# Kernel optimization log

Hardware: AMD Instinct MI355X
Metric: run time of the kernel (lower is better)

The kernel has to match this reference:

```python
import jax, jax.numpy as jnp
import numpy as np

DIM = 768
NH = 12
HD = DIM // NH
HIDDEN = 4 * DIM
Z_SIZE = (8, 8)
X_SIZE = (16, 16)
SCALE = HD ** -0.5
LN_EPS = 1e-5


def _rel_index(q_size, kv_size):
    hq, wq = q_size
    hk, wk = kv_size
    cq = np.stack(np.meshgrid(np.arange(hq), np.arange(wq), indexing='ij'), -1).reshape(-1, 2)
    ck = np.stack(np.meshgrid(np.arange(hk), np.arange(wk), indexing='ij'), -1).reshape(-1, 2)
    rel = cq[:, None, :] - ck[None, :, :]  # (Lq, Lk, 2)
    rel[..., 0] += hk - 1
    rel[..., 1] += wk - 1
    return jnp.asarray(rel[..., 0] * (wq + wk - 1) + rel[..., 1])  # (Lq, Lk)

ZX_IDX = _rel_index(Z_SIZE, X_SIZE)  # (64, 256)
XZ_IDX = _rel_index(X_SIZE, Z_SIZE)  # (256, 64)


def _ln(v, g, b):
    m = jnp.mean(v, -1, keepdims=True)
    var = jnp.var(v, -1, keepdims=True)
    return (v - m) * jax.lax.rsqrt(var + LN_EPS) * g + b


def _cross_attn(q_in, kv_in, qw, qb, kvw, kvb, pw, pb, rpb, idx):
    B, Lq, D = q_in.shape
    Lk = kv_in.shape[1]
    q = (q_in @ qw.T + qb).reshape(B, Lq, NH, HD).transpose(0, 2, 1, 3)  # (B,H,Lq,hd)
    kv = (kv_in @ kvw.T + kvb).reshape(B, Lk, 2, NH, HD).transpose(2, 0, 3, 1, 4)
    k, v = kv[0], kv[1]  # (B,H,Lk,hd)
    bias = rpb[idx].transpose(2, 0, 1)  # (H,Lq,Lk)
    attn = jnp.einsum('bhqd,bhkd->bhqk', q, k) * SCALE + bias[None]
    attn = jax.nn.softmax(attn, axis=-1)
    o = jnp.einsum('bhqk,bhkd->bhqd', attn, v).transpose(0, 2, 1, 3).reshape(B, Lq, D)
    return o @ pw.T + pb


def _mlp(v, w1, b1, w2, b2):
    return jax.nn.gelu(v @ w1.T + b1, approximate=False) @ w2.T + b2


def setup_inputs() -> dict:
    key = jax.random.key(0)
    ks = jax.random.split(key, 24)
    w = lambda k, s: jax.random.normal(k, s, jnp.float32) * 0.02
    TBL = (Z_SIZE[0] + X_SIZE[0] - 1) * (Z_SIZE[1] + X_SIZE[1] - 1)  # 529
    return {
        'z': jax.random.normal(ks[0], (64, 64, DIM), jnp.float32),
        'x': jax.random.normal(ks[1], (64, 256, DIM), jnp.float32),
        'z_ln1_g': jnp.ones((DIM,), jnp.float32), 'z_ln1_b': jnp.zeros((DIM,), jnp.float32),
        'x_ln1_g': jnp.ones((DIM,), jnp.float32), 'x_ln1_b': jnp.zeros((DIM,), jnp.float32),
        'zx_qw': w(ks[2], (DIM, DIM)), 'zx_qb': jnp.zeros((DIM,), jnp.float32),
        'zx_kvw': w(ks[3], (2 * DIM, DIM)), 'zx_kvb': jnp.zeros((2 * DIM,), jnp.float32),
        'zx_pw': w(ks[4], (DIM, DIM)), 'zx_pb': jnp.zeros((DIM,), jnp.float32),
        'zx_rpb': w(ks[5], (TBL, NH)),
        'xz_qw': w(ks[6], (DIM, DIM)), 'xz_qb': jnp.zeros((DIM,), jnp.float32),
        'xz_kvw': w(ks[7], (2 * DIM, DIM)), 'xz_kvb': jnp.zeros((2 * DIM,), jnp.float32),
        'xz_pw': w(ks[8], (DIM, DIM)), 'xz_pb': jnp.zeros((DIM,), jnp.float32),
        'xz_rpb': w(ks[9], (TBL, NH)),
        'z_ln2_g': jnp.ones((DIM,), jnp.float32), 'z_ln2_b': jnp.zeros((DIM,), jnp.float32),
        'z_fc1_w': w(ks[10], (HIDDEN, DIM)), 'z_fc1_b': jnp.zeros((HIDDEN,), jnp.float32),
        'z_fc2_w': w(ks[11], (DIM, HIDDEN)), 'z_fc2_b': jnp.zeros((DIM,), jnp.float32),
        'x_ln2_g': jnp.ones((DIM,), jnp.float32), 'x_ln2_b': jnp.zeros((DIM,), jnp.float32),
        'x_fc1_w': w(ks[12], (HIDDEN, DIM)), 'x_fc1_b': jnp.zeros((HIDDEN,), jnp.float32),
        'x_fc2_w': w(ks[13], (DIM, HIDDEN)), 'x_fc2_b': jnp.zeros((DIM,), jnp.float32),
    }


def reference(z, x, z_ln1_g, z_ln1_b, x_ln1_g, x_ln1_b,
              zx_qw, zx_qb, zx_kvw, zx_kvb, zx_pw, zx_pb, zx_rpb,
              xz_qw, xz_qb, xz_kvw, xz_kvb, xz_pw, xz_pb, xz_rpb,
              z_ln2_g, z_ln2_b, z_fc1_w, z_fc1_b, z_fc2_w, z_fc2_b,
              x_ln2_g, x_ln2_b, x_fc1_w, x_fc1_b, x_fc2_w, x_fc2_b):
    zn = _ln(z, z_ln1_g, z_ln1_b)
    xn = _ln(x, x_ln1_g, x_ln1_b)
    z_attn = _cross_attn(zn, xn, zx_qw, zx_qb, zx_kvw, zx_kvb, zx_pw, zx_pb, zx_rpb, ZX_IDX)
    x_attn = _cross_attn(xn, zn, xz_qw, xz_qb, xz_kvw, xz_kvb, xz_pw, xz_pb, xz_rpb, XZ_IDX)
    z2 = z + z_attn
    z2 = z2 + _mlp(_ln(z2, z_ln2_g, z_ln2_b), z_fc1_w, z_fc1_b, z_fc2_w, z_fc2_b)
    x2 = x + x_attn
    x2 = x2 + _mlp(_ln(x2, x_ln2_g, x_ln2_b), x_fc1_w, x_fc1_b, x_fc2_w, x_fc2_b)
    return (z2, x2)
```

## Files before the change

kernel.cpp:

```cpp
#include <hip/hip_runtime.h>
#include <math.h>

typedef unsigned short u16;
typedef unsigned int u32;
typedef __attribute__((ext_vector_type(8))) short bf16x8;
typedef __attribute__((ext_vector_type(4))) float f32x4;
typedef __attribute__((ext_vector_type(4))) u16 u16x4;

__device__ __forceinline__ u16 f2bf(float f) {
  u32 u = __builtin_bit_cast(u32, f);
  u32 r = (u + 0x7fffu + ((u >> 16) & 1u)) >> 16;
  return (u16)r;
}

__device__ __forceinline__ float gelu_f(float v) {
  float u = 1.5957691216057308f * v * (1.0f + 0.044715f * v * v);
  return v / (1.0f + __expf(-u));
}

__device__ __forceinline__ void async16(const void* g, void* l) {
  __builtin_amdgcn_global_load_lds(
      (__attribute__((address_space(1))) void*)(unsigned long long)(const char*)g,
      (__attribute__((address_space(3))) void*)l, 16, 0, 0);
}

#define SCHED0 __builtin_amdgcn_sched_barrier(0)
#define BARRIER __builtin_amdgcn_s_barrier()

struct Conv10 {
  const float* src[10];
  u16* dst[10];
  int n[10];
};

__global__ __launch_bounds__(256) void convert10(Conv10 a) {
  const int seg = blockIdx.y;
  const long i = ((long)blockIdx.x * 256 + threadIdx.x) * 4;
  if (i >= a.n[seg]) return;
  float4 v = *(const float4*)&a.src[seg][i];
  u16x4 o;
  o.x = f2bf(v.x); o.y = f2bf(v.y); o.z = f2bf(v.z); o.w = f2bf(v.w);
  *(u16x4*)&a.dst[seg][i] = o;
}

__global__ __launch_bounds__(256) void pack_bias(
    const float* __restrict__ zq, const float* __restrict__ zkv,
    const float* __restrict__ xq, const float* __restrict__ xkv,
    float* __restrict__ bz, float* __restrict__ bx)
{
  const int i = blockIdx.x * 256 + threadIdx.x;
  if (i >= 2304) return;
  bz[i] = (i < 768) ? zq[i] : zkv[i - 768];
  bx[i] = (i < 768) ? xq[i] : xkv[i - 768];
}

__global__ __launch_bounds__(256) void ln_dual(
    const float* __restrict__ in1, const float* __restrict__ g1, const float* __restrict__ b1,
    u16* __restrict__ out1, int rows1,
    const float* __restrict__ in2, const float* __restrict__ g2, const float* __restrict__ b2,
    u16* __restrict__ out2)
{
  const int w = threadIdx.x >> 6;
  const int lane = threadIdx.x & 63;
  const int row = blockIdx.x * 4 + w;
  const float* in; const float* gg; const float* bb; u16* out;
  if (row < rows1) { in = in1 + (size_t)row * 768; gg = g1; bb = b1; out = out1 + (size_t)row * 768; }
  else { const int r2 = row - rows1; in = in2 + (size_t)r2 * 768; gg = g2; bb = b2; out = out2 + (size_t)r2 * 768; }

  float4 v0 = *(const float4*)&in[lane * 4];
  float4 v1 = *(const float4*)&in[lane * 4 + 256];
  float4 v2 = *(const float4*)&in[lane * 4 + 512];
  float s = v0.x + v0.y + v0.z + v0.w + v1.x + v1.y + v1.z + v1.w + v2.x + v2.y + v2.z + v2.w;
  float s2 = v0.x*v0.x + v0.y*v0.y + v0.z*v0.z + v0.w*v0.w
           + v1.x*v1.x + v1.y*v1.y + v1.z*v1.z + v1.w*v1.w
           + v2.x*v2.x + v2.y*v2.y + v2.z*v2.z + v2.w*v2.w;
#pragma unroll
  for (int m = 1; m <= 32; m <<= 1) { s += __shfl_xor(s, m); s2 += __shfl_xor(s2, m); }
  const float mean = s * (1.0f / 768.0f);
  const float var = s2 * (1.0f / 768.0f) - mean * mean;
  const float rs = rsqrtf(var + 1e-5f);

#define LNSTORE(V, OFFS) { \
    float4 gv = *(const float4*)&gg[lane * 4 + OFFS]; \
    float4 bv = *(const float4*)&bb[lane * 4 + OFFS]; \
    u16x4 o; \
    o.x = f2bf((V.x - mean) * rs * gv.x + bv.x); \
    o.y = f2bf((V.y - mean) * rs * gv.y + bv.y); \
    o.z = f2bf((V.z - mean) * rs * gv.z + bv.z); \
    o.w = f2bf((V.w - mean) * rs * gv.w + bv.w); \
    *(u16x4*)&out[lane * 4 + OFFS] = o; }
  LNSTORE(v0, 0)
  LNSTORE(v1, 256)
  LNSTORE(v2, 512)
#undef LNSTORE
}

template<int EPI>
__device__ __forceinline__ void gemm5_core(
    const u16* __restrict__ A, const u16* __restrict__ W,
    const float* __restrict__ bias, const float* __restrict__ res,
    void* __restrict__ outp, long row0, long col0, int N, int K)
{
  __shared__ __align__(16) u16 As[3][256 * 32];
  __shared__ __align__(16) u16 Bs[3][128 * 32];

  const int tid = threadIdx.x;
  const int lane = tid & 63;
  const int w = tid >> 6;
  const int wm = w >> 1;
  const int wn = w & 1;

  const u16* gA[4];
  const u16* gB[2];
#pragma unroll
  for (int l = 0; l < 4; ++l) {
    const int e = l * 256 + tid;
    const int r = e >> 2, sl = e & 3;
    gA[l] = A + (row0 + r) * (long)K + ((sl ^ ((r >> 1) & 3)) * 8);
  }
#pragma unroll
  for (int l = 0; l < 2; ++l) {
    const int e = l * 256 + tid;
    const int r = e >> 2, sl = e & 3;
    gB[l] = W + (col0 + r) * (long)K + ((sl ^ ((r >> 1) & 3)) * 8);
  }

  const int fr = lane & 15;
  const int g = lane >> 4;

  f32x4 acc[8][4];
#pragma unroll
  for (int m = 0; m < 8; ++m)
#pragma unroll
    for (int n = 0; n < 4; ++n) acc[m][n] = (f32x4){0.f, 0.f, 0.f, 0.f};

  auto stage = [&](u16* ab, u16* bb, long ko) {
#pragma unroll
    for (int l = 0; l < 4; ++l) async16(gA[l] + ko, &ab[(l * 256 + tid) * 8]);
#pragma unroll
    for (int l = 0; l < 2; ++l) async16(gB[l] + ko, &bb[(l * 256 + tid) * 8]);
  };

  const int nt = K / 32;
  u16 *a0 = &As[0][0], *a1 = &As[1][0], *a2 = &As[2][0];
  u16 *b0 = &Bs[0][0], *b1 = &Bs[1][0], *b2 = &Bs[2][0];

  stage(a0, b0, 0);
  stage(a1, b1, 32);
  SCHED0;
  asm volatile("s_waitcnt vmcnt(6)" ::: "memory");
  BARRIER;
  SCHED0;

  for (int t = 0; t < nt; ++t) {
    if (t + 2 < nt) stage(a2, b2, (long)(t + 2) * 32);
    SCHED0;
    bf16x8 bfr[4];
#pragma unroll
    for (int n = 0; n < 4; ++n) {
      const int r = wn * 64 + n * 16 + fr;
      bfr[n] = *(const bf16x8*)&b0[r * 32 + ((g ^ ((r >> 1) & 3)) * 8)];
    }
    __builtin_amdgcn_s_setprio(1);
#pragma unroll
    for (int m = 0; m < 8; ++m) {
      const int r = wm * 128 + m * 16 + fr;
      bf16x8 af = *(const bf16x8*)&a0[r * 32 + ((g ^ ((r >> 1) & 3)) * 8)];
#pragma unroll
      for (int n = 0; n < 4; ++n)
        acc[m][n] = __builtin_amdgcn_mfma_f32_16x16x32_bf16(af, bfr[n], acc[m][n], 0, 0, 0);
    }
    __builtin_amdgcn_s_setprio(0);
    SCHED0;
    if (t + 2 < nt) {
      asm volatile("s_waitcnt vmcnt(6) lgkmcnt(0)" ::: "memory");
    } else if (t + 1 < nt) {
      asm volatile("s_waitcnt vmcnt(0) lgkmcnt(0)" ::: "memory");
    }
    if (t + 1 < nt) { BARRIER; SCHED0; }
    u16* ta = a0; a0 = a1; a1 = a2; a2 = ta;
    u16* tb = b0; b0 = b1; b1 = b2; b2 = tb;
  }

  float bv[4];
#pragma unroll
  for (int n = 0; n < 4; ++n) bv[n] = bias[col0 + wn * 64 + n * 16 + fr];
#pragma unroll
  for (int m = 0; m < 8; ++m) {
#pragma unroll
    for (int j = 0; j < 4; ++j) {
      const long row = row0 + wm * 128 + m * 16 + g * 4 + j;
      const long base = row * N + col0 + wn * 64 + fr;
#pragma unroll
      for (int n = 0; n < 4; ++n) {
        float v = acc[m][n][j] + bv[n];
        if constexpr (EPI == 0) {
          ((u16*)outp)[base + n * 16] = f2bf(v);
        } else if constexpr (EPI == 1) {
          ((u16*)outp)[base + n * 16] = f2bf(gelu_f(v));
        } else {
          ((float*)outp)[base + n * 16] = v + res[base + n * 16];
        }
      }
    }
  }
}

template<int EPI>
__global__ __launch_bounds__(256, 2) void gemm5(
    const u16* __restrict__ A, const u16* __restrict__ W,
    const float* __restrict__ bias, const float* __restrict__ res,
    void* __restrict__ outp, int M, int N, int K)
{
  int flat = blockIdx.y * gridDim.x + blockIdx.x;
  const int nwg = gridDim.x * gridDim.y;
  if ((nwg & 7) == 0) flat = (flat & 7) * (nwg >> 3) + (flat >> 3);
  const int bx = flat % gridDim.x;
  const int by = flat / gridDim.x;
  gemm5_core<EPI>(A, W, bias, res, outp, (long)by * 256, (long)bx * 128, N, K);
}

template<int EPI>
__global__ __launch_bounds__(256, 2) void gemm5f(
    const u16* __restrict__ A0, const u16* __restrict__ W0,
    const float* __restrict__ bias0, const float* __restrict__ res0, void* __restrict__ out0,
    const u16* __restrict__ A1, const u16* __restrict__ W1,
    const float* __restrict__ bias1, const float* __restrict__ res1, void* __restrict__ out1,
    int Y0, int N, int K)
{
  int flat = blockIdx.y * gridDim.x + blockIdx.x;
  const int nwg = gridDim.x * gridDim.y;
  if ((nwg & 7) == 0) flat = (flat & 7) * (nwg >> 3) + (flat >> 3);
  const int bx = flat % gridDim.x;
  const int by = flat / gridDim.x;
  if (by < Y0) {
    gemm5_core<EPI>(A0, W0, bias0, res0, out0, (long)by * 256, (long)bx * 128, N, K);
  } else {
    gemm5_core<EPI>(A1, W1, bias1, res1, out1, (long)(by - Y0) * 256, (long)bx * 128, N, K);
  }
}

template<int LQ>
__device__ __forceinline__ int rel_index(int q, int k) {
  if constexpr (LQ == 64) {
    const int qh = q >> 3, qw = q & 7, kh = k >> 4, kw = k & 15;
    return (qh - kh + 15) * 23 + (qw - kw + 15);
  } else {
    const int qh = q >> 4, qw = q & 15, kh = k >> 3, kw = k & 7;
    return (qh - kh + 7) * 23 + (qw - kw + 7);
  }
}

template<int LQ, int LK>
__global__ __launch_bounds__(256) void attn_kernel(
    const u16* __restrict__ Q, int qs, const u16* __restrict__ KV, int ks,
    const float* __restrict__ rpb, u16* __restrict__ O)
{
  constexpr int MT = LQ / 64;
  constexpr int NT = LK / 16;
  constexpr int KSPV = LK / 32;

  __shared__ __align__(16) u16 Qs[LQ * 64];
  __shared__ __align__(16) u16 Ks[LK * 64];
  __shared__ __align__(16) u16 Vt[64 * LK];
  __shared__ __align__(16) u16 Ps[LQ * LK];
  __shared__ float bias_s[529];

  const int h = blockIdx.x;
  const int b = blockIdx.y;
  const int tid = threadIdx.x;
  const int lane = tid & 63;
  const int w = tid >> 6;

  for (int i = tid; i < 529; i += 256) bias_s[i] = rpb[i * 12 + h];

#pragma unroll
  for (int it = 0; it < LQ * 8 / 256; ++it) {
    const int s = it * 256 + tid;
    const int r = s >> 3, sl2 = s & 7;
    bf16x8 v = *(const bf16x8*)&Q[(size_t)(b * LQ + r) * qs + h * 64 + sl2 * 8];
    *(bf16x8*)&Qs[r * 64 + ((sl2 ^ (r & 7)) * 8)] = v;
  }
#pragma unroll
  for (int it = 0; it < LK * 8 / 256; ++it) {
    const int s = it * 256 + tid;
    const int r = s >> 3, sl2 = s & 7;
    bf16x8 v = *(const bf16x8*)&KV[(size_t)(b * LK + r) * ks + h * 64 + sl2 * 8];
    *(bf16x8*)&Ks[r * 64 + ((sl2 ^ (r & 7)) * 8)] = v;
  }
#pragma unroll
  for (int it = 0; it < LK * 8 / 256; ++it) {
    const int s = it * 256 + tid;
    const int r = s >> 3, sl2 = s & 7;
    const int d0 = sl2 * 8;
    bf16x8 v = *(const bf16x8*)&KV[(size_t)(b * LK + r) * ks + 768 + h * 64 + d0];
#pragma unroll
    for (int j = 0; j < 8; ++j) {
      const int d = d0 + j;
      Vt[d * LK + (((r >> 3) ^ (d & 7)) * 8) + (r & 7)] = (u16)v[j];
    }
  }
  __syncthreads();

  const int fr = lane & 15;
  const int g = lane >> 4;
  const int qbase = w * MT * 16;

  f32x4 sacc[MT][NT];
#pragma unroll
  for (int mt = 0; mt < MT; ++mt)
#pragma unroll
    for (int nt = 0; nt < NT; ++nt) sacc[mt][nt] = (f32x4){0.f, 0.f, 0.f, 0.f};

#pragma unroll
  for (int mt = 0; mt < MT; ++mt) {
    const int qr = qbase + mt * 16 + fr;
    bf16x8 aq0 = *(const bf16x8*)&Qs[qr * 64 + (((0 + g) ^ (qr & 7)) * 8)];
    bf16x8 aq1 = *(const bf16x8*)&Qs[qr * 64 + (((4 + g) ^ (qr & 7)) * 8)];
#pragma unroll
    for (int nt = 0; nt < NT; ++nt) {
      const int kr = nt * 16 + fr;
      bf16x8 bk0 = *(const bf16x8*)&Ks[kr * 64 + (((0 + g) ^ (kr & 7)) * 8)];
      bf16x8 bk1 = *(const bf16x8*)&Ks[kr * 64 + (((4 + g) ^ (kr & 7)) * 8)];
      sacc[mt][nt] = __builtin_amdgcn_mfma_f32_16x16x32_bf16(aq0, bk0, sacc[mt][nt], 0, 0, 0);
      sacc[mt][nt] = __builtin_amdgcn_mfma_f32_16x16x32_bf16(aq1, bk1, sacc[mt][nt], 0, 0, 0);
    }
  }

#pragma unroll
  for (int mt = 0; mt < MT; ++mt) {
#pragma unroll
    for (int reg = 0; reg < 4; ++reg) {
      const int q = qbase + mt * 16 + g * 4 + reg;
      float mx = -3.0e38f;
#pragma unroll
      for (int nt = 0; nt < NT; ++nt) {
        const int k = nt * 16 + fr;
        float s = sacc[mt][nt][reg] * 0.125f + bias_s[rel_index<LQ>(q, k)];
        sacc[mt][nt][reg] = s;
        mx = fmaxf(mx, s);
      }
      mx = fmaxf(mx, __shfl_xor(mx, 1));
      mx = fmaxf(mx, __shfl_xor(mx, 2));
      mx = fmaxf(mx, __shfl_xor(mx, 4));
      mx = fmaxf(mx, __shfl_xor(mx, 8));
      float sum = 0.f;
#pragma unroll
      for (int nt = 0; nt < NT; ++nt) {
        float p = __expf(sacc[mt][nt][reg] - mx);
        sacc[mt][nt][reg] = p;
        sum += p;
      }
      sum += __shfl_xor(sum, 1);
      sum += __shfl_xor(sum, 2);
      sum += __shfl_xor(sum, 4);
      sum += __shfl_xor(sum, 8);
      const float inv = 1.0f / sum;
#pragma unroll
      for (int nt = 0; nt < NT; ++nt) {
        const int k = nt * 16 + fr;
        Ps[q * LK + (((k >> 3) ^ (q & 7)) * 8) + (k & 7)] = f2bf(sacc[mt][nt][reg] * inv);
      }
    }
  }
  __syncthreads();

  f32x4 oacc[MT][4];
#pragma unroll
  for (int mt = 0; mt < MT; ++mt)
#pragma unroll
    for (int n = 0; n < 4; ++n) oacc[mt][n] = (f32x4){0.f, 0.f, 0.f, 0.f};

#pragma unroll
  for (int mt = 0; mt < MT; ++mt) {
    const int pr = qbase + mt * 16 + fr;
#pragma unroll
    for (int ks2 = 0; ks2 < KSPV; ++ks2) {
      bf16x8 ap = *(const bf16x8*)&Ps[pr * LK + (((ks2 * 4 + g) ^ (pr & 7)) * 8)];
#pragma unroll
      for (int n = 0; n < 4; ++n) {
        const int d = n * 16 + fr;
        bf16x8 bvv = *(const bf16x8*)&Vt[d * LK + (((ks2 * 4 + g) ^ (d & 7)) * 8)];
        oacc[mt][n] = __builtin_amdgcn_mfma_f32_16x16x32_bf16(ap, bvv, oacc[mt][n], 0, 0, 0);
      }
    }
  }

#pragma unroll
  for (int mt = 0; mt < MT; ++mt)
#pragma unroll
    for (int n = 0; n < 4; ++n)
#pragma unroll
      for (int reg = 0; reg < 4; ++reg) {
        const int q = qbase + mt * 16 + g * 4 + reg;
        const int d = n * 16 + fr;
        O[(size_t)(b * LQ + q) * 768 + h * 64 + d] = f2bf(oacc[mt][n][reg]);
      }
}

extern "C" void kernel_launch(void* const* d_in, const int* in_sizes, int n_in,
                              void* d_out, int out_size, void* d_ws, size_t ws_size,
                              hipStream_t stream)
{
  const float* z      = (const float*)d_in[0];
  const float* x      = (const float*)d_in[1];
  const float* zln1g  = (const float*)d_in[2];
  const float* zln1b  = (const float*)d_in[3];
  const float* xln1g  = (const float*)d_in[4];
  const float* xln1b  = (const float*)d_in[5];
  const float* zx_qw  = (const float*)d_in[6];
  const float* zx_qb  = (const float*)d_in[7];
  const float* zx_kvw = (const float*)d_in[8];
  const float* zx_kvb = (const float*)d_in[9];
  const float* zx_pw  = (const float*)d_in[10];
  const float* zx_pb  = (const float*)d_in[11];
  const float* zx_rpb = (const float*)d_in[12];
  const float* xz_qw  = (const float*)d_in[13];
  const float* xz_qb  = (const float*)d_in[14];
  const float* xz_kvw = (const float*)d_in[15];
  const float* xz_kvb = (const float*)d_in[16];
  const float* xz_pw  = (const float*)d_in[17];
  const float* xz_pb  = (const float*)d_in[18];
  const float* xz_rpb = (const float*)d_in[19];
  const float* zln2g  = (const float*)d_in[20];
  const float* zln2b  = (const float*)d_in[21];
  const float* zfc1w  = (const float*)d_in[22];
  const float* zfc1b  = (const float*)d_in[23];
  const float* zfc2w  = (const float*)d_in[24];
  const float* zfc2b  = (const float*)d_in[25];
  const float* xln2g  = (const float*)d_in[26];
  const float* xln2b  = (const float*)d_in[27];
  const float* xfc1w  = (const float*)d_in[28];
  const float* xfc1b  = (const float*)d_in[29];
  const float* xfc2w  = (const float*)d_in[30];
  const float* xfc2b  = (const float*)d_in[31];

  float* out = (float*)d_out;
  float* z2 = out;
  float* x2 = out + 3145728;

  char* ws = (char*)d_ws;
  size_t off = 0;
  auto take = [&](size_t bytes) {
    char* p = ws + off;
    off += (bytes + 255) & ~(size_t)255;
    return p;
  };
  u16* w_zn   = (u16*)take(1769472 * 2);
  u16* w_xn   = (u16*)take(1769472 * 2);
  u16* w_zx_p = (u16*)take(589824 * 2);
  u16* w_xz_p = (u16*)take(589824 * 2);
  u16* w_zfc1 = (u16*)take(2359296 * 2);
  u16* w_zfc2 = (u16*)take(2359296 * 2);
  u16* w_xfc1 = (u16*)take(2359296 * 2);
  u16* w_xfc2 = (u16*)take(2359296 * 2);
  float* b_zn = (float*)take(2304 * 4);
  float* b_xn = (float*)take(2304 * 4);
  u16* regA   = (u16*)take(31457280);

  const size_t need_full = off + 125829120;
  const bool full = (ws_size >= need_full);
  u16* regB = (u16*)take(full ? 125829120 : 94371840);

  u16* zn    = regA;
  u16* xn    = regA + 3145728;
  u16* qkv_z = regB;
  u16* qkv_x = regB + 9437184;
  u16* ao_z  = zn;
  u16* ao_x  = xn;
  u16* z2n   = zn;
  u16* x2n   = xn;
  u16* hz    = regB;
  u16* hx    = regB + 12582912;

  Conv10 c;
  c.src[0] = zx_qw;  c.dst[0] = w_zn;           c.n[0] = 589824;
  c.src[1] = xz_kvw; c.dst[1] = w_zn + 589824;  c.n[1] = 1179648;
  c.src[2] = xz_qw;  c.dst[2] = w_xn;           c.n[2] = 589824;
  c.src[3] = zx_kvw; c.dst[3] = w_xn + 589824;  c.n[3] = 1179648;
  c.src[4] = zx_pw;  c.dst[4] = w_zx_p;         c.n[4] = 589824;
  c.src[5] = xz_pw;  c.dst[5] = w_xz_p;         c.n[5] = 589824;
  c.src[6] = zfc1w;  c.dst[6] = w_zfc1;         c.n[6] = 2359296;
  c.src[7] = zfc2w;  c.dst[7] = w_zfc2;         c.n[7] = 2359296;
  c.src[8] = xfc1w;  c.dst[8] = w_xfc1;         c.n[8] = 2359296;
  c.src[9] = xfc2w;  c.dst[9] = w_xfc2;         c.n[9] = 2359296;
  convert10<<<dim3(2304, 10), 256, 0, stream>>>(c);
  pack_bias<<<9, 256, 0, stream>>>(zx_qb, xz_kvb, xz_qb, zx_kvb, b_zn, b_xn);

  ln_dual<<<5120, 256, 0, stream>>>(z, zln1g, zln1b, zn, 4096, x, xln1g, xln1b, xn);

  gemm5f<0><<<dim3(18, 80), 256, 0, stream>>>(
      zn, w_zn, b_zn, nullptr, qkv_z,
      xn, w_xn, b_xn, nullptr, qkv_x, 16, 2304, 768);

  attn_kernel<64, 256><<<dim3(12, 64), 256, 0, stream>>>(qkv_z, 2304, qkv_x + 768, 2304, zx_rpb, ao_z);
  attn_kernel<256, 64><<<dim3(12, 64), 256, 0, stream>>>(qkv_x, 2304, qkv_z + 768, 2304, xz_rpb, ao_x);

  gemm5f<2><<<dim3(6, 80), 256, 0, stream>>>(
      ao_z, w_zx_p, zx_pb, z, z2,
      ao_x, w_xz_p, xz_pb, x, x2, 16, 768, 768);

  ln_dual<<<5120, 256, 0, stream>>>(z2, zln2g, zln2b, z2n, 4096, x2, xln2g, xln2b, x2n);

  if (full) {
    gemm5f<1><<<dim3(24, 80), 256, 0, stream>>>(
        z2n, w_zfc1, zfc1b, nullptr, hz,
        x2n, w_xfc1, xfc1b, nullptr, hx, 16, 3072, 768);
    gemm5f<2><<<dim3(6, 80), 256, 0, stream>>>(
        hz, w_zfc2, zfc2b, z2, z2,
        hx, w_xfc2, xfc2b, x2, x2, 16, 768, 3072);
  } else {
    gemm5f<1><<<dim3(24, 48), 256, 0, stream>>>(
        z2n, w_zfc1, zfc1b, nullptr, hz,
        x2n, w_xfc1, xfc1b, nullptr, hx, 16, 3072, 768);
    gemm5f<2><<<dim3(6, 48), 256, 0, stream>>>(
        hz, w_zfc2, zfc2b, z2, z2,
        hx, w_xfc2, xfc2b, x2, x2, 16, 768, 3072);
    gemm5<1><<<dim3(24, 32), 256, 0, stream>>>(x2n + (size_t)8192 * 768, w_xfc1, xfc1b, nullptr, hx, 8192, 3072, 768);
    gemm5<2><<<dim3(6, 32),  256, 0, stream>>>(hx, w_xfc2, xfc2b, x2 + (size_t)8192 * 768, x2 + (size_t)8192 * 768, 8192, 768, 3072);
  }
}
```

Before: 569.7 us.

## Switch GEMM to 32x32x16 MFMA and merge prep and attention launches

The GEMM core moves from 16x16x32 MFMA tiles to 32x32x16 tiles, so fewer LDS fragment reads are needed per MFMA and the epilogue store mapping changes to match. Weight conversion, bias packing and the first layernorm are merged into one prep kernel, and the two attention launches become one launch that uses blockIdx.z with dynamically carved shared memory. The aim is higher matrix-core throughput and fewer launches. The costs are a larger shared buffer for the attention kernel, sized for the bigger of the two shapes, and a changed output store pattern that may coalesce less well.

```diff
diff --git a/kernel.cpp b/kernel.cpp
--- a/kernel.cpp
+++ b/kernel.cpp
@@ -5,6 +5,7 @@
 typedef unsigned int u32;
 typedef __attribute__((ext_vector_type(8))) short bf16x8;
 typedef __attribute__((ext_vector_type(4))) float f32x4;
+typedef __attribute__((ext_vector_type(16))) float f32x16;
 typedef __attribute__((ext_vector_type(4))) u16 u16x4;
 
 __device__ __forceinline__ u16 f2bf(float f) {
@@ -27,45 +28,18 @@
 #define SCHED0 __builtin_amdgcn_sched_barrier(0)
 #define BARRIER __builtin_amdgcn_s_barrier()
 
-struct Conv10 {
-  const float* src[10];
-  u16* dst[10];
-  int n[10];
-};
-
-__global__ __launch_bounds__(256) void convert10(Conv10 a) {
-  const int seg = blockIdx.y;
-  const long i = ((long)blockIdx.x * 256 + threadIdx.x) * 4;
-  if (i >= a.n[seg]) return;
-  float4 v = *(const float4*)&a.src[seg][i];
-  u16x4 o;
-  o.x = f2bf(v.x); o.y = f2bf(v.y); o.z = f2bf(v.z); o.w = f2bf(v.w);
-  *(u16x4*)&a.dst[seg][i] = o;
-}
-
-__global__ __launch_bounds__(256) void pack_bias(
-    const float* __restrict__ zq, const float* __restrict__ zkv,
-    const float* __restrict__ xq, const float* __restrict__ xkv,
-    float* __restrict__ bz, float* __restrict__ bx)
-{
-  const int i = blockIdx.x * 256 + threadIdx.x;
-  if (i >= 2304) return;
-  bz[i] = (i < 768) ? zq[i] : zkv[i - 768];
-  bx[i] = (i < 768) ? xq[i] : xkv[i - 768];
-}
-
-__global__ __launch_bounds__(256) void ln_dual(
+__device__ __forceinline__ void ln_rows4(
     const float* __restrict__ in1, const float* __restrict__ g1, const float* __restrict__ b1,
     u16* __restrict__ out1, int rows1,
-    const float* __restrict__ in2, const float* __restrict__ g2, const float* __restrict__ b2,
-    u16* __restrict__ out2)
+    const float* __restrict__ in2, const float* __restrict__ g2v, const float* __restrict__ b2v,
+    u16* __restrict__ out2, int rowblk)
 {
   const int w = threadIdx.x >> 6;
   const int lane = threadIdx.x & 63;
-  const int row = blockIdx.x * 4 + w;
+  const int row = rowblk * 4 + w;
   const float* in; const float* gg; const float* bb; u16* out;
   if (row < rows1) { in = in1 + (size_t)row * 768; gg = g1; bb = b1; out = out1 + (size_t)row * 768; }
-  else { const int r2 = row - rows1; in = in2 + (size_t)r2 * 768; gg = g2; bb = b2; out = out2 + (size_t)r2 * 768; }
+  else { const int r2 = row - rows1; in = in2 + (size_t)r2 * 768; gg = g2v; bb = b2v; out = out2 + (size_t)r2 * 768; }
 
   float4 v0 = *(const float4*)&in[lane * 4];
   float4 v1 = *(const float4*)&in[lane * 4 + 256];
@@ -95,6 +69,43 @@
 #undef LNSTORE
 }
 
+__global__ __launch_bounds__(256) void ln_dual(
+    const float* __restrict__ in1, const float* __restrict__ g1, const float* __restrict__ b1,
+    u16* __restrict__ out1, int rows1,
+    const float* __restrict__ in2, const float* __restrict__ g2, const float* __restrict__ b2,
+    u16* __restrict__ out2)
+{
+  ln_rows4(in1, g1, b1, out1, rows1, in2, g2, b2, out2, blockIdx.x);
+}
+
+struct PrepArgs {
+  const float* csrc[10]; u16* cdst[10]; int cn[10];
+  const float* z; const float* zg; const float* zb; u16* zo;
+  const float* x; const float* xg; const float* xb; u16* xo;
+  const float* zq; const float* zkv; const float* xq; const float* xkv;
+  float* bz; float* bx;
+};
+
+__global__ __launch_bounds__(256) void prep(PrepArgs a) {
+  const int b = blockIdx.x;
+  if (b < 23040) {
+    const int seg = b / 2304;
+    const long i = ((long)(b % 2304) * 256 + threadIdx.x) * 4;
+    if (i >= a.cn[seg]) return;
+    float4 v = *(const float4*)&a.csrc[seg][i];
+    u16x4 o;
+    o.x = f2bf(v.x); o.y = f2bf(v.y); o.z = f2bf(v.z); o.w = f2bf(v.w);
+    *(u16x4*)&a.cdst[seg][i] = o;
+  } else if (b < 28160) {
+    ln_rows4(a.z, a.zg, a.zb, a.zo, 4096, a.x, a.xg, a.xb, a.xo, b - 23040);
+  } else {
+    const int i = (b - 28160) * 256 + threadIdx.x;
+    if (i >= 2304) return;
+    a.bz[i] = (i < 768) ? a.zq[i] : a.zkv[i - 768];
+    a.bx[i] = (i < 768) ? a.xq[i] : a.xkv[i - 768];
+  }
+}
+
 template<int EPI>
 __device__ __forceinline__ void gemm5_core(
     const u16* __restrict__ A, const u16* __restrict__ W,
@@ -125,14 +136,16 @@
     gB[l] = W + (col0 + r) * (long)K + ((sl ^ ((r >> 1) & 3)) * 8);
   }
 
-  const int fr = lane & 15;
-  const int g = lane >> 4;
-
-  f32x4 acc[8][4];
-#pragma unroll
-  for (int m = 0; m < 8; ++m)
-#pragma unroll
-    for (int n = 0; n < 4; ++n) acc[m][n] = (f32x4){0.f, 0.f, 0.f, 0.f};
+  const int r32 = lane & 31;
+  const int g2 = lane >> 5;
+
+  f32x16 acc[4][2];
+#pragma unroll
+  for (int mf = 0; mf < 4; ++mf)
+#pragma unroll
+    for (int nf = 0; nf < 2; ++nf)
+#pragma unroll
+      for (int q = 0; q < 16; ++q) acc[mf][nf][q] = 0.f;
 
   auto stage = [&](u16* ab, u16* bb, long ko) {
 #pragma unroll
@@ -155,20 +168,25 @@
   for (int t = 0; t < nt; ++t) {
     if (t + 2 < nt) stage(a2, b2, (long)(t + 2) * 32);
     SCHED0;
-    bf16x8 bfr[4];
-#pragma unroll
-    for (int n = 0; n < 4; ++n) {
-      const int r = wn * 64 + n * 16 + fr;
-      bfr[n] = *(const bf16x8*)&b0[r * 32 + ((g ^ ((r >> 1) & 3)) * 8)];
+    bf16x8 bfr[2][2];
+#pragma unroll
+    for (int nf = 0; nf < 2; ++nf) {
+      const int r = wn * 64 + nf * 32 + r32;
+#pragma unroll
+      for (int kk = 0; kk < 2; ++kk)
+        bfr[nf][kk] = *(const bf16x8*)&b0[r * 32 + (((kk * 2 + g2) ^ ((r >> 1) & 3)) * 8)];
     }
     __builtin_amdgcn_s_setprio(1);
 #pragma unroll
-    for (int m = 0; m < 8; ++m) {
-      const int r = wm * 128 + m * 16 + fr;
-      bf16x8 af = *(const bf16x8*)&a0[r * 32 + ((g ^ ((r >> 1) & 3)) * 8)];
-#pragma unroll
-      for (int n = 0; n < 4; ++n)
-        acc[m][n] = __builtin_amdgcn_mfma_f32_16x16x32_bf16(af, bfr[n], acc[m][n], 0, 0, 0);
+    for (int mf = 0; mf < 4; ++mf) {
+      const int r = wm * 128 + mf * 32 + r32;
+#pragma unroll
+      for (int kk = 0; kk < 2; ++kk) {
+        bf16x8 af = *(const bf16x8*)&a0[r * 32 + (((kk * 2 + g2) ^ ((r >> 1) & 3)) * 8)];
+#pragma unroll
+        for (int nf = 0; nf < 2; ++nf)
+          acc[mf][nf] = __builtin_amdgcn_mfma_f32_32x32x16_bf16(af, bfr[nf][kk], acc[mf][nf], 0, 0, 0);
+      }
     }
     __builtin_amdgcn_s_setprio(0);
     SCHED0;
@@ -182,24 +200,24 @@
     u16* tb = b0; b0 = b1; b1 = b2; b2 = tb;
   }
 
-  float bv[4];
-#pragma unroll
-  for (int n = 0; n < 4; ++n) bv[n] = bias[col0 + wn * 64 + n * 16 + fr];
-#pragma unroll
-  for (int m = 0; m < 8; ++m) {
-#pragma unroll
-    for (int j = 0; j < 4; ++j) {
-      const long row = row0 + wm * 128 + m * 16 + g * 4 + j;
-      const long base = row * N + col0 + wn * 64 + fr;
-#pragma unroll
-      for (int n = 0; n < 4; ++n) {
-        float v = acc[m][n][j] + bv[n];
+  float bv[2];
+#pragma unroll
+  for (int nf = 0; nf < 2; ++nf) bv[nf] = bias[col0 + wn * 64 + nf * 32 + r32];
+#pragma unroll
+  for (int mf = 0; mf < 4; ++mf) {
+#pragma unroll
+    for (int rg = 0; rg < 16; ++rg) {
+      const long row = row0 + wm * 128 + mf * 32 + (rg & 3) + 8 * (rg >> 2) + 4 * g2;
+      const long base = row * N + col0 + wn * 64 + r32;
+#pragma unroll
+      for (int nf = 0; nf < 2; ++nf) {
+        float v = acc[mf][nf][rg] + bv[nf];
         if constexpr (EPI == 0) {
-          ((u16*)outp)[base + n * 16] = f2bf(v);
+          ((u16*)outp)[base + nf * 32] = f2bf(v);
         } else if constexpr (EPI == 1) {
-          ((u16*)outp)[base + n * 16] = f2bf(gelu_f(v));
+          ((u16*)outp)[base + nf * 32] = f2bf(gelu_f(v));
         } else {
-          ((float*)outp)[base + n * 16] = v + res[base + n * 16];
+          ((float*)outp)[base + nf * 32] = v + res[base + nf * 32];
         }
       }
     }
@@ -252,22 +270,20 @@
 }
 
 template<int LQ, int LK>
-__global__ __launch_bounds__(256) void attn_kernel(
+__device__ void attn_core(
     const u16* __restrict__ Q, int qs, const u16* __restrict__ KV, int ks,
-    const float* __restrict__ rpb, u16* __restrict__ O)
+    const float* __restrict__ rpb, u16* __restrict__ O, char* sm, int h, int b)
 {
   constexpr int MT = LQ / 64;
   constexpr int NT = LK / 16;
   constexpr int KSPV = LK / 32;
 
-  __shared__ __align__(16) u16 Qs[LQ * 64];
-  __shared__ __align__(16) u16 Ks[LK * 64];
-  __shared__ __align__(16) u16 Vt[64 * LK];
-  __shared__ __align__(16) u16 Ps[LQ * LK];
-  __shared__ float bias_s[529];
-
-  const int h = blockIdx.x;
-  const int b = blockIdx.y;
+  u16* Qs = (u16*)sm;
+  u16* Ks = Qs + LQ * 64;
+  u16* Vt = Ks + LK * 64;
+  u16* Ps = Vt + 64 * LK;
+  float* bias_s = (float*)(Ps + (size_t)LQ * LK);
+
   const int tid = threadIdx.x;
   const int lane = tid & 63;
   const int w = tid >> 6;
@@ -396,6 +412,19 @@
         const int d = n * 16 + fr;
         O[(size_t)(b * LQ + q) * 768 + h * 64 + d] = f2bf(oacc[mt][n][reg]);
       }
+}
+
+__global__ __launch_bounds__(256) void attn_both(
+    const u16* __restrict__ qkv_z, const u16* __restrict__ qkv_x,
+    const float* __restrict__ zx_rpb, const float* __restrict__ xz_rpb,
+    u16* __restrict__ ao_z, u16* __restrict__ ao_x)
+{
+  __shared__ __align__(16) char sm[108624];
+  const int h = blockIdx.x, b = blockIdx.y;
+  if (blockIdx.z == 0)
+    attn_core<64, 256>(qkv_z, 2304, qkv_x + 768, 2304, zx_rpb, ao_z, sm, h, b);
+  else
+    attn_core<256, 64>(qkv_x, 2304, qkv_z + 768, 2304, xz_rpb, ao_x, sm, h, b);
 }
 
 extern "C" void kernel_launch(void* const* d_in, const int* in_sizes, int n_in,
@@ -473,28 +502,28 @@
   u16* hz    = regB;
   u16* hx    = regB + 12582912;
 
-  Conv10 c;
-  c.src[0] = zx_qw;  c.dst[0] = w_zn;           c.n[0] = 589824;
-  c.src[1] = xz_kvw; c.dst[1] = w_zn + 589824;  c.n[1] = 1179648;
-  c.src[2] = xz_qw;  c.dst[2] = w_xn;           c.n[2] = 589824;
-  c.src[3] = zx_kvw; c.dst[3] = w_xn + 589824;  c.n[3] = 1179648;
-  c.src[4] = zx_pw;  c.dst[4] = w_zx_p;         c.n[4] = 589824;
-  c.src[5] = xz_pw;  c.dst[5] = w_xz_p;         c.n[5] = 589824;
-  c.src[6] = zfc1w;  c.dst[6] = w_zfc1;         c.n[6] = 2359296;
-  c.src[7] = zfc2w;  c.dst[7] = w_zfc2;         c.n[7] = 2359296;
-  c.src[8] = xfc1w;  c.dst[8] = w_xfc1;         c.n[8] = 2359296;
-  c.src[9] = xfc2w;  c.dst[9] = w_xfc2;         c.n[9] = 2359296;
-  convert10<<<dim3(2304, 10), 256, 0, stream>>>(c);
-  pack_bias<<<9, 256, 0, stream>>>(zx_qb, xz_kvb, xz_qb, zx_kvb, b_zn, b_xn);
-
-  ln_dual<<<5120, 256, 0, stream>>>(z, zln1g, zln1b, zn, 4096, x, xln1g, xln1b, xn);
+  PrepArgs a;
+  a.csrc[0] = zx_qw;  a.cdst[0] = w_zn;           a.cn[0] = 589824;
+  a.csrc[1] = xz_kvw; a.cdst[1] = w_zn + 589824;  a.cn[1] = 1179648;
+  a.csrc[2] = xz_qw;  a.cdst[2] = w_xn;           a.cn[2] = 589824;
+  a.csrc[3] = zx_kvw; a.cdst[3] = w_xn + 589824;  a.cn[3] = 1179648;
+  a.csrc[4] = zx_pw;  a.cdst[4] = w_zx_p;         a.cn[4] = 589824;
+  a.csrc[5] = xz_pw;  a.cdst[5] = w_xz_p;         a.cn[5] = 589824;
+  a.csrc[6] = zfc1w;  a.cdst[6] = w_zfc1;         a.cn[6] = 2359296;
+  a.csrc[7] = zfc2w;  a.cdst[7] = w_zfc2;         a.cn[7] = 2359296;
+  a.csrc[8] = xfc1w;  a.cdst[8] = w_xfc1;         a.cn[8] = 2359296;
+  a.csrc[9] = xfc2w;  a.cdst[9] = w_xfc2;         a.cn[9] = 2359296;
+  a.z = z; a.zg = zln1g; a.zb = zln1b; a.zo = zn;
+  a.x = x; a.xg = xln1g; a.xb = xln1b; a.xo = xn;
+  a.zq = zx_qb; a.zkv = xz_kvb; a.xq = xz_qb; a.xkv = zx_kvb;
+  a.bz = b_zn; a.bx = b_xn;
+  prep<<<28169, 256, 0, stream>>>(a);
 
   gemm5f<0><<<dim3(18, 80), 256, 0, stream>>>(
       zn, w_zn, b_zn, nullptr, qkv_z,
       xn, w_xn, b_xn, nullptr, qkv_x, 16, 2304, 768);
 
-  attn_kernel<64, 256><<<dim3(12, 64), 256, 0, stream>>>(qkv_z, 2304, qkv_x + 768, 2304, zx_rpb, ao_z);
-  attn_kernel<256, 64><<<dim3(12, 64), 256, 0, stream>>>(qkv_x, 2304, qkv_z + 768, 2304, xz_rpb, ao_x);
+  attn_both<<<dim3(12, 64, 2), 256, 0, stream>>>(qkv_z, qkv_x, zx_rpb, xz_rpb, ao_z, ao_x);
 
   gemm5f<2><<<dim3(6, 80), 256, 0, stream>>>(
       ao_z, w_zx_p, zx_pb, z, z2,
```

Measured after the change: 591.6 us. +3.8%, slower.
